# Kernel optimization log

Hardware: AMD Instinct MI355X
Metric: run time of the kernel (lower is better)

Reference implementation:

```python
import jax, jax.numpy as jnp
import numpy as np

SAT_LO, SAT_HI = -1.0, 1.0  # args_dict['saturations']


def setup_inputs() -> dict:
    key = jax.random.key(0)
    ks = jax.random.split(key, 6)
    B, T, n = 256, 512, 1024
    std = 1.0 / np.sqrt(n)
    x = jax.random.normal(ks[0], (B, T), jnp.float32)
    state0 = jnp.zeros((n,), jnp.float32)
    mask = jnp.ones((n,), jnp.float32)
    # 2x2 recurrent mixing matrix, scaled roughly to spectral radius ~init_radius
    w = 0.9 * jax.random.normal(ks[1], (2, 2), jnp.float32) * std * np.sqrt(n)
    dec_orth = jax.random.normal(ks[2], (n,), jnp.float32) * std
    enc_orth = jax.random.normal(ks[3], (n,), jnp.float32) * std
    decoder = jax.random.normal(ks[4], (n,), jnp.float32) * std
    encoder = jax.random.normal(ks[5], (n,), jnp.float32) * std
    return {"x": x, "state0": state0, "mask": mask, "w": w,
            "dec_orth": dec_orth, "enc_orth": enc_orth,
            "decoder": decoder, "encoder": encoder}


def reference(x, state0, mask, w, dec_orth, enc_orth, decoder, encoder):
    # W = sum_ij w[i,j] * v_i (x) v_j with v_0 = dec_orth, v_1 = enc_orth  -> [n, n]
    W = (w[0, 0] * jnp.outer(dec_orth, dec_orth)
         + w[0, 1] * jnp.outer(dec_orth, enc_orth)
         + w[1, 0] * jnp.outer(enc_orth, dec_orth)
         + w[1, 1] * jnp.outer(enc_orth, enc_orth))
    B = x.shape[0]
    n = state0.shape[0]
    s0 = jnp.zeros((B, n), x.dtype) + state0  # broadcast init state to batch

    def step(s, xt):
        # external current: encoder * x_t  -> [B, n]
        pre = (s + mask * (encoder * xt[:, None])) @ W.T
        s_new = mask * jnp.clip(pre, SAT_LO, SAT_HI)
        out = s_new @ decoder  # [B]
        return s_new, out

    _, outs = jax.lax.scan(step, s0, x.T)  # outs: [T, B]
    return outs.T  # [B, T]
```

## Files before the change

kernel.cpp:

```cpp
#include <hip/hip_runtime.h>


typedef float f32x2 __attribute__((ext_vector_type(2)));

constexpr int Bc = 256;
constexpr int Tc = 512;
constexpr int CH = Tc / 64;

template <int CTRL, int RMASK>
__device__ __forceinline__ float dpp_add(float v) {
    int t = __builtin_amdgcn_update_dpp(0, __float_as_int(v), CTRL, RMASK, 0xf, true);
    return v + __int_as_float(t);
}

__device__ __forceinline__ float wave_sum63(float v) {
    v = dpp_add<0x111, 0xf>(v);
    v = dpp_add<0x112, 0xf>(v);
    v = dpp_add<0x114, 0xf>(v);
    v = dpp_add<0x118, 0xf>(v);
    v = dpp_add<0x142, 0xa>(v);
    v = dpp_add<0x143, 0xc>(v);
    return v;
}

__device__ __forceinline__ float readlane_f(float v, int l) {
    return __int_as_float(__builtin_amdgcn_readlane(__float_as_int(v), l));
}

__device__ __forceinline__ f32x2 pk_fma(f32x2 a, f32x2 b, f32x2 c) {
    f32x2 d;
    asm("v_pk_fma_f32 %0, %1, %2, %3" : "=v"(d) : "v"(a), "v"(b), "v"(c));
    return d;
}

__device__ __forceinline__ f32x2 pk_mul(f32x2 a, f32x2 b) {
    f32x2 d;
    asm("v_pk_mul_f32 %0, %1, %2" : "=v"(d) : "v"(a), "v"(b));
    return d;
}

#define DECL_TBL(i) f32x2 d2_##i, e2_##i, g1_##i, g2_##i, wo_##i

#define INIT_TBL(i) do { \
    _Pragma("unroll") \
    for (int h = 0; h < 2; ++h) { \
        const int c = lane + 64 * (2 * (i) + h); \
        const float dv   = dec_orth[c]; \
        const float ev   = enc_orth[c]; \
        const float mv   = mask[c]; \
        const float encv = encoder[c]; \
        const float decv = decoder[c]; \
        const float s0v  = state0[c]; \
        const float mdv = mv * dv, mev = mv * ev; \
        d2_##i[h]  = dv;  e2_##i[h]  = ev; \
        g1_##i[h] = fmaf(w00, mdv, w01 * mev); \
        g2_##i[h] = fmaf(w10, mdv, w11 * mev); \
        wo_##i[h] = mv * decv; \
        s0d += s0v * dv;  s0e += s0v * ev; \
        kd = fmaf(mv * encv, dv, kd); \
        ke = fmaf(mv * encv, ev, ke); \
    } \
} while (0)

#define PIN_TBL(i) \
    asm volatile("" : "+v"(d2_##i), "+v"(e2_##i), "+v"(g1_##i), "+v"(g2_##i), "+v"(wo_##i))

#define ACC_PAIR(i, OP1, OP2, OP3) do { \
    f32x2 tt = pk_fma(r2, e2_##i, d2_##i); \
    f32x2 mm; \
    mm.x = __builtin_amdgcn_fmed3f(tt.x, nb, bb); \
    mm.y = __builtin_amdgcn_fmed3f(tt.y, nb, bb); \
    OP1; OP2; OP3; \
} while (0)

__global__ __launch_bounds__(64, 1) void twotwonet_kernel(
    const float* __restrict__ x,
    const float* __restrict__ state0,
    const float* __restrict__ mask,
    const float* __restrict__ w,
    const float* __restrict__ dec_orth,
    const float* __restrict__ enc_orth,
    const float* __restrict__ decoder,
    const float* __restrict__ encoder,
    float* __restrict__ out)
{
    const int b    = blockIdx.x;
    const int lane = threadIdx.x;

    const float w00 = w[0], w01 = w[1], w10 = w[2], w11 = w[3];

    DECL_TBL(0); DECL_TBL(1); DECL_TBL(2); DECL_TBL(3);
    DECL_TBL(4); DECL_TBL(5); DECL_TBL(6); DECL_TBL(7);

    float s0d = 0.f, s0e = 0.f, kd = 0.f, ke = 0.f;
    INIT_TBL(0); INIT_TBL(1); INIT_TBL(2); INIT_TBL(3);
    INIT_TBL(4); INIT_TBL(5); INIT_TBL(6); INIT_TBL(7);

    PIN_TBL(0); PIN_TBL(1); PIN_TBL(2); PIN_TBL(3);
    PIN_TBL(4); PIN_TBL(5); PIN_TBL(6); PIN_TBL(7);

#pragma unroll
    for (int m = 32; m >= 1; m >>= 1) {
        s0d += __shfl_xor(s0d, m, 64);
        s0e += __shfl_xor(s0e, m, 64);
        kd  += __shfl_xor(kd, m, 64);
        ke  += __shfl_xor(ke, m, 64);
    }

    const float A1 = fmaf(w00, kd, w01 * ke);
    const float A2 = fmaf(w10, kd, w11 * ke);

    const float* xrow = x + (size_t)b * Tc;
    float xr[CH];
#pragma unroll
    for (int c = 0; c < CH; ++c) xr[c] = xrow[lane + 64 * c];
    asm volatile("" : "+v"(xr[0]), "+v"(xr[1]), "+v"(xr[2]), "+v"(xr[3]),
                      "+v"(xr[4]), "+v"(xr[5]), "+v"(xr[6]), "+v"(xr[7]));

    float au = 1.0f;
    float q1 = fmaf(w00, s0d, w01 * s0e);
    float q2 = fmaf(w10, s0d, w11 * s0e);

#pragma unroll
    for (int c = 0; c < CH; ++c) {
        float obuf = 0.f;
#pragma unroll 2
        for (int t2 = 0; t2 < 64; ++t2) {
            const float xs = readlane_f(xr[c], t2);

            const float alpha = fmaf(au, q1, xs * A1);
            const float beta  = fmaf(au, q2, xs * A2);

            const float aun = copysignf(fmaxf(fabsf(alpha), 1e-20f), alpha);
            const float inv = __builtin_amdgcn_rcpf(aun);
            const float r   = beta * inv;
            const float bb  = fabsf(inv);
            const float nb  = -bb;
            const f32x2 r2  = {r, r};

            f32x2 a1a, a1b, a2a, a2b, aoa, aob;
            ACC_PAIR(0, a1a = pk_mul(mm, g1_0), a2a = pk_mul(mm, g2_0), aoa = pk_mul(mm, wo_0));
            ACC_PAIR(1, a1a = pk_fma(mm, g1_1, a1a), a2a = pk_fma(mm, g2_1, a2a), aoa = pk_fma(mm, wo_1, aoa));
            ACC_PAIR(2, a1a = pk_fma(mm, g1_2, a1a), a2a = pk_fma(mm, g2_2, a2a), aoa = pk_fma(mm, wo_2, aoa));
            ACC_PAIR(3, a1a = pk_fma(mm, g1_3, a1a), a2a = pk_fma(mm, g2_3, a2a), aoa = pk_fma(mm, wo_3, aoa));
            ACC_PAIR(4, a1b = pk_mul(mm, g1_4), a2b = pk_mul(mm, g2_4), aob = pk_mul(mm, wo_4));
            ACC_PAIR(5, a1b = pk_fma(mm, g1_5, a1b), a2b = pk_fma(mm, g2_5, a2b), aob = pk_fma(mm, wo_5, aob));
            ACC_PAIR(6, a1b = pk_fma(mm, g1_6, a1b), a2b = pk_fma(mm, g2_6, a2b), aob = pk_fma(mm, wo_6, aob));
            ACC_PAIR(7, a1b = pk_fma(mm, g1_7, a1b), a2b = pk_fma(mm, g2_7, a2b), aob = pk_fma(mm, wo_7, aob));

            const f32x2 s1v = a1a + a1b;
            const f32x2 s2v = a2a + a2b;
            const f32x2 sov = aoa + aob;
            float h1 = s1v.x + s1v.y;
            float h2 = s2v.x + s2v.y;
            float ho = sov.x + sov.y;

            h1 = wave_sum63(h1);
            h2 = wave_sum63(h2);
            ho = wave_sum63(ho);

            q1 = readlane_f(h1, 63);
            q2 = readlane_f(h2, 63);
            const float so = readlane_f(ho, 63);
            au = aun;

            const float ov = aun * so;
            obuf = (t2 == lane) ? ov : obuf;
        }
        out[(size_t)b * Tc + 64 * c + lane] = obuf;
    }
}

extern "C" void kernel_launch(void* const* d_in, const int* in_sizes, int n_in,
                              void* d_out, int out_size, void* d_ws, size_t ws_size,
                              hipStream_t stream) {
    const float* x        = (const float*)d_in[0];
    const float* state0   = (const float*)d_in[1];
    const float* mask     = (const float*)d_in[2];
    const float* w        = (const float*)d_in[3];
    const float* dec_orth = (const float*)d_in[4];
    const float* enc_orth = (const float*)d_in[5];
    const float* decoder  = (const float*)d_in[6];
    const float* encoder  = (const float*)d_in[7];
    float* out = (float*)d_out;

    twotwonet_kernel<<<dim3(Bc), dim3(64), 0, stream>>>(
        x, state0, mask, w, dec_orth, enc_orth, decoder, encoder, out);
}
```

Baseline: 117.8 us.

## Drop rcp-normalized recurrence, use direct clamp and fused inline-asm DPP reductions

Replaces the scaled recurrence, which kept a running alpha and used a reciprocal plus a ratio with a variable clamp bound, with the direct form: each element is clamped to [-1,1] from al*d + be*e. The three wave reductions and their readlanes move into one inline-asm block that interleaves the DPP adds of the three sums, removing the compiler's separate reduction chains. The register-pinning asm barriers are dropped and waves_per_eu is set to 1. This removes the rcp and scaling from the serial critical path but adds one packed multiply per pair, and the hand-written DPP sequence relies on the s_nop placement being enough for hazards.

```diff
diff --git a/kernel.cpp b/kernel.cpp
--- a/kernel.cpp
+++ b/kernel.cpp
@@ -6,22 +6,6 @@
 constexpr int Bc = 256;
 constexpr int Tc = 512;
 constexpr int CH = Tc / 64;
-
-template <int CTRL, int RMASK>
-__device__ __forceinline__ float dpp_add(float v) {
-    int t = __builtin_amdgcn_update_dpp(0, __float_as_int(v), CTRL, RMASK, 0xf, true);
-    return v + __int_as_float(t);
-}
-
-__device__ __forceinline__ float wave_sum63(float v) {
-    v = dpp_add<0x111, 0xf>(v);
-    v = dpp_add<0x112, 0xf>(v);
-    v = dpp_add<0x114, 0xf>(v);
-    v = dpp_add<0x118, 0xf>(v);
-    v = dpp_add<0x142, 0xa>(v);
-    v = dpp_add<0x143, 0xc>(v);
-    return v;
-}
 
 __device__ __forceinline__ float readlane_f(float v, int l) {
     return __int_as_float(__builtin_amdgcn_readlane(__float_as_int(v), l));
@@ -32,12 +16,30 @@
     asm("v_pk_fma_f32 %0, %1, %2, %3" : "=v"(d) : "v"(a), "v"(b), "v"(c));
     return d;
 }
-
 __device__ __forceinline__ f32x2 pk_mul(f32x2 a, f32x2 b) {
     f32x2 d;
     asm("v_pk_mul_f32 %0, %1, %2" : "=v"(d) : "v"(a), "v"(b));
     return d;
 }
+
+#define DPP3(lvl, msk)                                                                              \
+        "v_add_f32_dpp %[a], %[a], %[a] " lvl " row_mask:" msk " bank_mask:0xf bound_ctrl:1\n\t"    \
+        "v_add_f32_dpp %[b], %[b], %[b] " lvl " row_mask:" msk " bank_mask:0xf bound_ctrl:1\n\t"    \
+        "v_add_f32_dpp %[c], %[c], %[c] " lvl " row_mask:" msk " bank_mask:0xf bound_ctrl:1\n\t"
+
+#define WAVE_REDUCE3_READ(h1, h2, h3, s1, s2, s3)                                                   \
+    asm("s_nop 1\n\t"                                                                               \
+        DPP3("row_shr:1",   "0xf")                                                                  \
+        DPP3("row_shr:2",   "0xf")                                                                  \
+        DPP3("row_shr:4",   "0xf")                                                                  \
+        DPP3("row_shr:8",   "0xf")                                                                  \
+        DPP3("row_bcast:15","0xa")                                                                  \
+        DPP3("row_bcast:31","0xc")                                                                  \
+        "v_readlane_b32 %[x], %[a], 63\n\t"                                                         \
+        "v_readlane_b32 %[y], %[b], 63\n\t"                                                         \
+        "v_readlane_b32 %[z], %[c], 63"                                                             \
+        : [a] "+v"(h1), [b] "+v"(h2), [c] "+v"(h3),                                                 \
+          [x] "=s"(s1), [y] "=s"(s2), [z] "=s"(s3))
 
 #define DECL_TBL(i) f32x2 d2_##i, e2_##i, g1_##i, g2_##i, wo_##i
 
@@ -62,18 +64,28 @@
     } \
 } while (0)
 
-#define PIN_TBL(i) \
-    asm volatile("" : "+v"(d2_##i), "+v"(e2_##i), "+v"(g1_##i), "+v"(g2_##i), "+v"(wo_##i))
-
-#define ACC_PAIR(i, OP1, OP2, OP3) do { \
-    f32x2 tt = pk_fma(r2, e2_##i, d2_##i); \
+#define ACC_J(i) do { \
+    f32x2 tt = pk_fma(b2, e2_##i, pk_mul(a2, d2_##i)); \
     f32x2 mm; \
-    mm.x = __builtin_amdgcn_fmed3f(tt.x, nb, bb); \
-    mm.y = __builtin_amdgcn_fmed3f(tt.y, nb, bb); \
-    OP1; OP2; OP3; \
+    mm.x = __builtin_amdgcn_fmed3f(tt.x, -1.0f, 1.0f); \
+    mm.y = __builtin_amdgcn_fmed3f(tt.y, -1.0f, 1.0f); \
+    p1 = pk_fma(mm, g1_##i, p1); \
+    p2 = pk_fma(mm, g2_##i, p2); \
+    po = pk_fma(mm, wo_##i, po); \
 } while (0)
 
-__global__ __launch_bounds__(64, 1) void twotwonet_kernel(
+#define ACC_J0(i) do { \
+    f32x2 tt = pk_fma(b2, e2_##i, pk_mul(a2, d2_##i)); \
+    f32x2 mm; \
+    mm.x = __builtin_amdgcn_fmed3f(tt.x, -1.0f, 1.0f); \
+    mm.y = __builtin_amdgcn_fmed3f(tt.y, -1.0f, 1.0f); \
+    p1 = pk_mul(mm, g1_##i); \
+    p2 = pk_mul(mm, g2_##i); \
+    po = pk_mul(mm, wo_##i); \
+} while (0)
+
+__global__ __attribute__((amdgpu_waves_per_eu(1, 1))) __launch_bounds__(64)
+void twotwonet_kernel(
     const float* __restrict__ x,
     const float* __restrict__ state0,
     const float* __restrict__ mask,
@@ -96,9 +108,6 @@
     INIT_TBL(0); INIT_TBL(1); INIT_TBL(2); INIT_TBL(3);
     INIT_TBL(4); INIT_TBL(5); INIT_TBL(6); INIT_TBL(7);
 
-    PIN_TBL(0); PIN_TBL(1); PIN_TBL(2); PIN_TBL(3);
-    PIN_TBL(4); PIN_TBL(5); PIN_TBL(6); PIN_TBL(7);
-
 #pragma unroll
     for (int m = 32; m >= 1; m >>= 1) {
         s0d += __shfl_xor(s0d, m, 64);
@@ -114,10 +123,7 @@
     float xr[CH];
 #pragma unroll
     for (int c = 0; c < CH; ++c) xr[c] = xrow[lane + 64 * c];
-    asm volatile("" : "+v"(xr[0]), "+v"(xr[1]), "+v"(xr[2]), "+v"(xr[3]),
-                      "+v"(xr[4]), "+v"(xr[5]), "+v"(xr[6]), "+v"(xr[7]));
 
-    float au = 1.0f;
     float q1 = fmaf(w00, s0d, w01 * s0e);
     float q2 = fmaf(w10, s0d, w11 * s0e);
 
@@ -128,44 +134,26 @@
         for (int t2 = 0; t2 < 64; ++t2) {
             const float xs = readlane_f(xr[c], t2);
 
-            const float alpha = fmaf(au, q1, xs * A1);
-            const float beta  = fmaf(au, q2, xs * A2);
+            const float al = fmaf(xs, A1, q1);
+            const float be = fmaf(xs, A2, q2);
+            const f32x2 a2 = {al, al};
+            const f32x2 b2 = {be, be};
 
-            const float aun = copysignf(fmaxf(fabsf(alpha), 1e-20f), alpha);
-            const float inv = __builtin_amdgcn_rcpf(aun);
-            const float r   = beta * inv;
-            const float bb  = fabsf(inv);
-            const float nb  = -bb;
-            const f32x2 r2  = {r, r};
+            f32x2 p1, p2, po;
+            ACC_J0(0);
+            ACC_J(1); ACC_J(2); ACC_J(3);
+            ACC_J(4); ACC_J(5); ACC_J(6); ACC_J(7);
 
-            f32x2 a1a, a1b, a2a, a2b, aoa, aob;
-            ACC_PAIR(0, a1a = pk_mul(mm, g1_0), a2a = pk_mul(mm, g2_0), aoa = pk_mul(mm, wo_0));
-            ACC_PAIR(1, a1a = pk_fma(mm, g1_1, a1a), a2a = pk_fma(mm, g2_1, a2a), aoa = pk_fma(mm, wo_1, aoa));
-            ACC_PAIR(2, a1a = pk_fma(mm, g1_2, a1a), a2a = pk_fma(mm, g2_2, a2a), aoa = pk_fma(mm, wo_2, aoa));
-            ACC_PAIR(3, a1a = pk_fma(mm, g1_3, a1a), a2a = pk_fma(mm, g2_3, a2a), aoa = pk_fma(mm, wo_3, aoa));
-            ACC_PAIR(4, a1b = pk_mul(mm, g1_4), a2b = pk_mul(mm, g2_4), aob = pk_mul(mm, wo_4));
-            ACC_PAIR(5, a1b = pk_fma(mm, g1_5, a1b), a2b = pk_fma(mm, g2_5, a2b), aob = pk_fma(mm, wo_5, aob));
-            ACC_PAIR(6, a1b = pk_fma(mm, g1_6, a1b), a2b = pk_fma(mm, g2_6, a2b), aob = pk_fma(mm, wo_6, aob));
-            ACC_PAIR(7, a1b = pk_fma(mm, g1_7, a1b), a2b = pk_fma(mm, g2_7, a2b), aob = pk_fma(mm, wo_7, aob));
+            float h1 = p1.x + p1.y;
+            float h2 = p2.x + p2.y;
+            float ho = po.x + po.y;
 
-            const f32x2 s1v = a1a + a1b;
-            const f32x2 s2v = a2a + a2b;
-            const f32x2 sov = aoa + aob;
-            float h1 = s1v.x + s1v.y;
-            float h2 = s2v.x + s2v.y;
-            float ho = sov.x + sov.y;
+            float r1, r2, ro;
+            WAVE_REDUCE3_READ(h1, h2, ho, r1, r2, ro);
+            q1 = r1;
+            q2 = r2;
 
-            h1 = wave_sum63(h1);
-            h2 = wave_sum63(h2);
-            ho = wave_sum63(ho);
-
-            q1 = readlane_f(h1, 63);
-            q2 = readlane_f(h2, 63);
-            const float so = readlane_f(ho, 63);
-            au = aun;
-
-            const float ov = aun * so;
-            obuf = (t2 == lane) ? ov : obuf;
+            obuf = (t2 == lane) ? ro : obuf;
         }
         out[(size_t)b * Tc + 64 * c + lane] = obuf;
     }
```

Measured after the change: 101.2 us. 1.16x faster.
